# Optimization experiments

Hardware: AMD Instinct MI355X
Metric: run time of the kernel (lower is better)

## Reference

```python
import jax, jax.numpy as jnp
import numpy as np

B, S, E, H = 2, 2048, 1024, 16
HD = E // H  # head_dim = 64


def setup_inputs() -> dict:
    key = jax.random.key(0)
    k_x, k_wqkv, k_bqkv, k_wo, k_bo = jax.random.split(key, 5)
    # nn.Linear-style init scale ~ 1/sqrt(fan_in)
    s = 1.0 / np.sqrt(E)
    return {
        "x": jax.random.normal(k_x, (B, S, E), dtype=jnp.float32),
        "W_qkv": jax.random.uniform(k_wqkv, (3 * E, E), jnp.float32, -s, s),
        "b_qkv": jax.random.uniform(k_bqkv, (3 * E,), jnp.float32, -s, s),
        "W_out": jax.random.uniform(k_wo, (E, E), jnp.float32, -s, s),
        "b_out": jax.random.uniform(k_bo, (E,), jnp.float32, -s, s),
    }


def reference(x, W_qkv, b_qkv, W_out, b_out):
    # Fused QKV projection: (B,S,E) -> (B,S,3E)
    qkv = jnp.einsum("bse,fe->bsf", x, W_qkv) + b_qkv
    # Faithful to the torch code: reshape to (B,S,H,3*HD), then chunk last dim.
    qkv = qkv.reshape(B, S, H, 3 * HD)
    q, k, v = jnp.split(qkv, 3, axis=-1)  # each (B,S,H,HD)
    scale = 1.0 / jnp.sqrt(jnp.asarray(HD, dtype=x.dtype))
    # scores: (B,H,S,S)
    scores = jnp.einsum("bshd,bthd->bhst", q, k) * scale
    weights = jax.nn.softmax(scores, axis=-1)
    # context: (B,S,H,HD) -> (B,S,E)
    ctx = jnp.einsum("bhst,bthd->bshd", weights, v).reshape(B, S, E)
    return jnp.einsum("bse,fe->bsf", ctx, W_out) + b_out
```

## Files before the change

kernel.cpp:

```cpp
#include <hip/hip_runtime.h>
#include <hip/hip_bf16.h>

#define B_  2
#define S_  2048
#define E_  1024
#define H_  16
#define HD_ 64
#define T_  (B_*S_)
#define F_  (3*E_)

#define SW(r)  ((((r) & 7) << 4) ^ (((r) & 8) << 2))
#define SWV(r) (((((r) & 7) ^ (((r) >> 4) & 3)) << 4) ^ (((r) & 8) << 2))

using bf16 = __hip_bfloat16;
typedef __attribute__((ext_vector_type(8))) short bf16x8;
typedef __attribute__((ext_vector_type(4))) short short4v;
typedef __attribute__((ext_vector_type(4))) float f32x4;
typedef __attribute__((ext_vector_type(16))) float f32x16;
typedef __attribute__((ext_vector_type(4))) int i32x4;
typedef __attribute__((ext_vector_type(2))) unsigned int u32x2;

__device__ inline short f2bf(float x) {
  __hip_bfloat16 h = __float2bfloat16(x);
  return __builtin_bit_cast(short, h);
}
__device__ inline float bf2f(short x) {
  return __bfloat162float(__builtin_bit_cast(__hip_bfloat16, x));
}
__device__ inline int pk2(float lo, float hig) {
  return (int)((unsigned short)f2bf(lo) |
               ((unsigned int)(unsigned short)f2bf(hig) << 16));
}

__device__ inline void gload_lds16(const void* g, void* l) {
  __builtin_amdgcn_global_load_lds(
      (const __attribute__((address_space(1))) void*)g,
      (__attribute__((address_space(3))) void*)l, 16, 0, 0);
}

__global__ __launch_bounds__(256) void cvt_f32_bf16(
    const float* __restrict__ in, short* __restrict__ out, int n8) {
  int i = blockIdx.x * 256 + threadIdx.x;
  if (i >= n8) return;
  const float4* p = (const float4*)in + (size_t)i * 2;
  float4 a = p[0], b = p[1];
  bf16x8 r;
  r[0] = f2bf(a.x); r[1] = f2bf(a.y); r[2] = f2bf(a.z); r[3] = f2bf(a.w);
  r[4] = f2bf(b.x); r[5] = f2bf(b.y); r[6] = f2bf(b.z); r[7] = f2bf(b.w);
  *(bf16x8*)(out + (size_t)i * 8) = r;
}

__device__ inline void store_out(short* p, float v) { *p = f2bf(v); }
__device__ inline void store_out(float* p, float v) { *p = v; }

template<typename OutT>
__global__ __launch_bounds__(256) void gemm_nt(
    const short* __restrict__ A,
    const short* __restrict__ Bm,
    const float* __restrict__ bias,
    OutT* __restrict__ C,
    int M, int N, int K) {
  __shared__ __align__(16) char sAB[32768];
  char* sA = sAB;
  char* sB = sAB + 16384;
  const int tid  = threadIdx.x;
  const int w    = tid >> 6, lane = tid & 63;
  const int lr   = lane & 15, g = lane >> 4;
  const int brow = blockIdx.y * 128, bcol = blockIdx.x * 128;
  const int wr   = (w >> 1) * 64,  wc   = (w & 1) * 64;

  f32x4 acc[4][4];
  #pragma unroll
  for (int i = 0; i < 4; ++i)
    #pragma unroll
    for (int j = 0; j < 4; ++j) acc[i][j] = (f32x4)0.0f;

  const size_t Kb = (size_t)K * 2;
  const char* Ag = (const char*)A + (size_t)brow * Kb;
  const char* Bg = (const char*)Bm + (size_t)bcol * Kb;

  for (int k0 = 0; k0 < K; k0 += 64) {
    #pragma unroll
    for (int i = 0; i < 4; ++i) {
      int base = i * 4096 + w * 1024;
      int lb   = base + lane * 16;
      int r    = lb >> 7;
      int cb   = (lb & 127) ^ ((r & 7) << 4);
      gload_lds16(Ag + (size_t)r * Kb + (size_t)k0 * 2 + cb, sA + base);
      gload_lds16(Bg + (size_t)r * Kb + (size_t)k0 * 2 + cb, sB + base);
    }
    __syncthreads();
    #pragma unroll
    for (int ks = 0; ks < 2; ++ks) {
      bf16x8 af[4], bfr[4];
      #pragma unroll
      for (int m = 0; m < 4; ++m) {
        int row = wr + m * 16 + lr;
        int cb  = (ks * 64 + g * 16) ^ ((row & 7) << 4);
        af[m] = *(const bf16x8*)(sA + row * 128 + cb);
      }
      #pragma unroll
      for (int n = 0; n < 4; ++n) {
        int row = wc + n * 16 + lr;
        int cb  = (ks * 64 + g * 16) ^ ((row & 7) << 4);
        bfr[n] = *(const bf16x8*)(sB + row * 128 + cb);
      }
      #pragma unroll
      for (int m = 0; m < 4; ++m)
        #pragma unroll
        for (int n = 0; n < 4; ++n)
          acc[m][n] = __builtin_amdgcn_mfma_f32_16x16x32_bf16(
              af[m], bfr[n], acc[m][n], 0, 0, 0);
    }
    __syncthreads();
  }
  #pragma unroll
  for (int n = 0; n < 4; ++n) {
    int f = bcol + wc + n * 16 + lr;
    float bv = bias[f];
    #pragma unroll
    for (int m = 0; m < 4; ++m) {
      int t0 = brow + wr + m * 16 + g * 4;
      #pragma unroll
      for (int j = 0; j < 4; ++j) {
        store_out(&C[(size_t)(t0 + j) * N + f], acc[m][n][j] + bv);
      }
    }
  }
}

__global__ __launch_bounds__(256) void gemm_nt_n64(
    const short* __restrict__ A,
    const short* __restrict__ Bm,
    const float* __restrict__ bias,
    float* __restrict__ C,
    int M, int N, int K) {
  __shared__ __align__(16) char sAB[24576];
  char* sA = sAB;
  char* sB = sAB + 16384;
  const int tid  = threadIdx.x;
  const int w    = tid >> 6, lane = tid & 63;
  const int lr   = lane & 15, g = lane >> 4;
  const int brow = blockIdx.y * 128, bcol = blockIdx.x * 64;

  f32x4 acc[2][4];
  #pragma unroll
  for (int i = 0; i < 2; ++i)
    #pragma unroll
    for (int j = 0; j < 4; ++j) acc[i][j] = (f32x4)0.0f;

  const size_t Kb = (size_t)K * 2;
  const char* Ag = (const char*)A + (size_t)brow * Kb;
  const char* Bg = (const char*)Bm + (size_t)bcol * Kb;

  for (int k0 = 0; k0 < K; k0 += 64) {
    #pragma unroll
    for (int i = 0; i < 4; ++i) {
      int base = i * 4096 + w * 1024;
      int lb   = base + lane * 16;
      int r    = lb >> 7;
      int cb   = (lb & 127) ^ ((r & 7) << 4);
      gload_lds16(Ag + (size_t)r * Kb + (size_t)k0 * 2 + cb, sA + base);
    }
    #pragma unroll
    for (int i = 0; i < 2; ++i) {
      int base = i * 4096 + w * 1024;
      int lb   = base + lane * 16;
      int r    = lb >> 7;
      int cb   = (lb & 127) ^ ((r & 7) << 4);
      gload_lds16(Bg + (size_t)r * Kb + (size_t)k0 * 2 + cb, sB + base);
    }
    __syncthreads();
    #pragma unroll
    for (int ks = 0; ks < 2; ++ks) {
      bf16x8 af[2], bfr[4];
      #pragma unroll
      for (int m = 0; m < 2; ++m) {
        int row = w * 32 + m * 16 + lr;
        int cb  = (ks * 64 + g * 16) ^ ((row & 7) << 4);
        af[m] = *(const bf16x8*)(sA + row * 128 + cb);
      }
      #pragma unroll
      for (int n = 0; n < 4; ++n) {
        int row = n * 16 + lr;
        int cb  = (ks * 64 + g * 16) ^ ((row & 7) << 4);
        bfr[n] = *(const bf16x8*)(sB + row * 128 + cb);
      }
      #pragma unroll
      for (int m = 0; m < 2; ++m)
        #pragma unroll
        for (int n = 0; n < 4; ++n)
          acc[m][n] = __builtin_amdgcn_mfma_f32_16x16x32_bf16(
              af[m], bfr[n], acc[m][n], 0, 0, 0);
    }
    __syncthreads();
  }
  #pragma unroll
  for (int n = 0; n < 4; ++n) {
    int f = bcol + n * 16 + lr;
    float bv = bias[f];
    #pragma unroll
    for (int m = 0; m < 2; ++m) {
      int t0 = brow + w * 32 + m * 16 + g * 4;
      #pragma unroll
      for (int j = 0; j < 4; ++j) {
        C[(size_t)(t0 + j) * N + f] = acc[m][n][j] + bv;
      }
    }
  }
}

__global__ __launch_bounds__(256) void attn_kernel(
    const short* __restrict__ qkv, short* __restrict__ ctx) {
  __shared__ __align__(16) char smem[32768];
  const int tid = threadIdx.x;
  const int w = tid >> 6, lane = tid & 63;
  const int ql = lane & 31, hi = lane >> 5;
  const int qblk = blockIdx.x, h = blockIdx.y, b = blockIdx.z;

  const size_t rowB = (size_t)F_ * 2;
  const char* base = (const char*)qkv + (size_t)b * S_ * rowB + (size_t)h * 384;

  const int qrow = qblk * 128 + w * 32 + ql;
  const char* qp = base + (size_t)qrow * rowB;
  bf16x8 qf[4];
  #pragma unroll
  for (int ks = 0; ks < 4; ++ks) {
    bf16x8 t = *(const bf16x8*)(qp + ks * 32 + hi * 16);
    #pragma unroll
    for (int j = 0; j < 8; ++j) t[j] = f2bf(bf2f(t[j]) * 0.180336880f);
    qf[ks] = t;
  }

  const int vkg = tid >> 4;
  const int vfg = tid & 15;
  const int vkgp = (vkg & 12) | ((vkg & 1) << 1) | ((vkg >> 1) & 1);

  float l_run = 0.0f;
  f32x16 ot0 = (f32x16)0.0f, ot1 = (f32x16)0.0f;

#define STAGE_K(dstoff, srcb)                                           \
  do {                                                                  \
    _Pragma("unroll")                                                   \
    for (int i = 0; i < 2; ++i) {                                       \
      int lbase = i * 4096 + w * 1024;                                  \
      int lb = lbase + lane * 16;                                       \
      int r  = lb >> 7;                                                 \
      int cb = (lb & 127) ^ SW(r);                                      \
      gload_lds16((srcb) + (size_t)r * rowB + 128 + cb,                 \
                  smem + (dstoff) + lbase);                             \
    }                                                                   \
  } while (0)

#define LOAD_V(srcb)                                                    \
  do {                                                                  \
    const char* vp_ = (srcb) + 256 + vfg * 8;                           \
    nv0 = *(const short4v*)(vp_ + (size_t)(vkg * 4 + 0) * rowB);        \
    nv1 = *(const short4v*)(vp_ + (size_t)(vkg * 4 + 1) * rowB);        \
    nv2 = *(const short4v*)(vp_ + (size_t)(vkg * 4 + 2) * rowB);        \
    nv3 = *(const short4v*)(vp_ + (size_t)(vkg * 4 + 3) * rowB);        \
  } while (0)

#define WRITE_VT(dstoff)                                                \
  do {                                                                  \
    char* dvt_ = smem + (dstoff) + 8192;                                \
    _Pragma("unroll")                                                   \
    for (int f = 0; f < 4; ++f) {                                       \
      int fr = vfg * 4 + f;                                             \
      u32x2 dw;                                                         \
      dw[0] = (unsigned short)nv0[f] |                                  \
              ((unsigned int)(unsigned short)nv1[f] << 16);             \
      dw[1] = (unsigned short)nv2[f] |                                  \
              ((unsigned int)(unsigned short)nv3[f] << 16);             \
      *(u32x2*)(dvt_ + fr * 128 + ((vkgp * 8) ^ SWV(fr))) = dw;         \
    }                                                                   \
  } while (0)

  {
    short4v nv0, nv1, nv2, nv3;
    STAGE_K(0, base);
    LOAD_V(base);
    WRITE_VT(0);
  }
  __syncthreads();

  int cur = 0;
  for (int kt = 0; kt < 32; ++kt) {
    const int nxt = cur ^ 1;
    const char* sK  = smem + cur * 16384;
    const char* sVt = sK + 8192;

    short4v nv0, nv1, nv2, nv3;
    const char* nkvb = base + (size_t)((kt + 1) * 64) * rowB;
    if (kt < 31) {
      STAGE_K(nxt * 16384, nkvb);
      LOAD_V(nkvb);
    }

    f32x16 st0 = (f32x16)0.0f, st1 = (f32x16)0.0f;
    __builtin_amdgcn_s_setprio(1);
    #pragma unroll
    for (int ks = 0; ks < 4; ++ks) {
      int cb = (ks * 32 + hi * 16) ^ SW(ql);
      bf16x8 k0 = *(const bf16x8*)(sK + ql * 128 + cb);
      bf16x8 k1 = *(const bf16x8*)(sK + (ql + 32) * 128 + cb);
      st0 = __builtin_amdgcn_mfma_f32_32x32x16_bf16(k0, qf[ks], st0, 0, 0, 0);
      st1 = __builtin_amdgcn_mfma_f32_32x32x16_bf16(k1, qf[ks], st1, 0, 0, 0);
    }
    __builtin_amdgcn_s_setprio(0);

    float p0[16], p1[16];
    float rs = 0.0f;
    #pragma unroll
    for (int r = 0; r < 16; ++r) {
      p0[r] = exp2f(st0[r]);
      p1[r] = exp2f(st1[r]);
      rs += p0[r] + p1[r];
    }
    l_run += rs;

    i32x4 paw[4];
    #pragma unroll
    for (int q = 0; q < 4; ++q) {
      paw[0][q] = pk2(p0[2 * q], p0[2 * q + 1]);
      paw[1][q] = pk2(p0[8 + 2 * q], p0[9 + 2 * q]);
      paw[2][q] = pk2(p1[2 * q], p1[2 * q + 1]);
      paw[3][q] = pk2(p1[8 + 2 * q], p1[9 + 2 * q]);
    }

    __builtin_amdgcn_s_setprio(1);
    #pragma unroll
    for (int ks = 0; ks < 4; ++ks) {
      int cb = (ks * 32 + hi * 16);
      bf16x8 pf = __builtin_bit_cast(bf16x8, paw[ks]);
      bf16x8 v0 = *(const bf16x8*)(sVt + ql * 128 + (cb ^ SWV(ql)));
      bf16x8 v1 = *(const bf16x8*)(sVt + (ql + 32) * 128 + (cb ^ SWV(ql + 32)));
      ot0 = __builtin_amdgcn_mfma_f32_32x32x16_bf16(v0, pf, ot0, 0, 0, 0);
      ot1 = __builtin_amdgcn_mfma_f32_32x32x16_bf16(v1, pf, ot1, 0, 0, 0);
    }
    __builtin_amdgcn_s_setprio(0);

    if (kt < 31) {
      WRITE_VT(nxt * 16384);
    }
    __syncthreads();
    cur = nxt;
  }

  l_run += __shfl_xor(l_run, 32);
  float inv = 1.0f / l_run;
  short* crow = ctx + ((size_t)b * S_ + qrow) * E_ + h * 64;
  #pragma unroll
  for (int i = 0; i < 8; ++i) {
    int f0 = ((2 * i) & 3) + 8 * (i >> 1) + 4 * hi;
    int w0 = pk2(ot0[2 * i] * inv, ot0[2 * i + 1] * inv);
    int w1 = pk2(ot1[2 * i] * inv, ot1[2 * i + 1] * inv);
    *(int*)(crow + f0)      = w0;
    *(int*)(crow + f0 + 32) = w1;
  }
#undef STAGE_K
#undef LOAD_V
#undef WRITE_VT
}

extern "C" void kernel_launch(void* const* d_in, const int* in_sizes, int n_in,
                              void* d_out, int out_size, void* d_ws, size_t ws_size,
                              hipStream_t stream) {
  const float* x    = (const float*)d_in[0];
  const float* Wqkv = (const float*)d_in[1];
  const float* bqkv = (const float*)d_in[2];
  const float* Wout = (const float*)d_in[3];
  const float* bout = (const float*)d_in[4];

  char* ws = (char*)d_ws;
  short* xb    = (short*)(ws);
  short* wqkvb = (short*)(ws + 8388608);
  short* woutb = (short*)(ws + 8388608 + 6291456);
  short* qkvb  = (short*)(ws + 16777216);
  short* ctx   = (short*)(ws + 16777216 + 25165824);

  cvt_f32_bf16<<<2048, 256, 0, stream>>>(x, xb, (T_ * E_) / 8);
  cvt_f32_bf16<<<1536, 256, 0, stream>>>(Wqkv, wqkvb, (F_ * E_) / 8);
  cvt_f32_bf16<<<512, 256, 0, stream>>>(Wout, woutb, (E_ * E_) / 8);

  gemm_nt<short><<<dim3(F_ / 128, T_ / 128), 256, 0, stream>>>(
      xb, wqkvb, bqkv, qkvb, T_, F_, E_);

  attn_kernel<<<dim3(S_ / 128, H_, B_), 256, 0, stream>>>(qkvb, ctx);

  gemm_nt_n64<<<dim3(E_ / 64, T_ / 128), 256, 0, stream>>>(
      ctx, woutb, bout, (float*)d_out, T_, E_, E_);
}
```

Baseline: 212.9 us.

## Triple-buffer K/V in attention with explicit waitcnts and merge convert kernels

The attention kernel moves from double to triple buffering of K/V tiles in LDS (48KB). K is prefetched two tiles ahead via direct global-to-LDS loads and V one tile ahead, and __syncthreads is replaced with manual s_waitcnt vmcnt/lgkmcnt plus s_barrier so later loads can stay in flight across the barrier. Separately, the three fp32-to-bf16 conversion launches are merged into one kernel writing a contiguous workspace region. The larger LDS footprint may lower occupancy, and the hand-written waitcnt counts depend on exactly how many memory ops each macro issues, which the compiler does not check.

Measured after the change: 210.4 us. About the same (-1.2%).

```diff
diff --git a/kernel.cpp b/kernel.cpp
--- a/kernel.cpp
+++ b/kernel.cpp
@@ -38,11 +38,19 @@
       (__attribute__((address_space(3))) void*)l, 16, 0, 0);
 }
 
-__global__ __launch_bounds__(256) void cvt_f32_bf16(
-    const float* __restrict__ in, short* __restrict__ out, int n8) {
+#define NX8 ((T_*E_)/8)
+#define NW8 ((F_*E_)/8)
+#define NO8 ((E_*E_)/8)
+__global__ __launch_bounds__(256) void cvt_all(
+    const float* __restrict__ x, const float* __restrict__ wqkv,
+    const float* __restrict__ wout, short* __restrict__ out) {
   int i = blockIdx.x * 256 + threadIdx.x;
-  if (i >= n8) return;
-  const float4* p = (const float4*)in + (size_t)i * 2;
+  const float* src;
+  int off;
+  if (i < NX8)            { src = x;    off = i; }
+  else if (i < NX8 + NW8) { src = wqkv; off = i - NX8; }
+  else                    { src = wout; off = i - NX8 - NW8; }
+  const float4* p = (const float4*)src + (size_t)off * 2;
   float4 a = p[0], b = p[1];
   bf16x8 r;
   r[0] = f2bf(a.x); r[1] = f2bf(a.y); r[2] = f2bf(a.z); r[3] = f2bf(a.w);
@@ -212,7 +220,7 @@
 
 __global__ __launch_bounds__(256) void attn_kernel(
     const short* __restrict__ qkv, short* __restrict__ ctx) {
-  __shared__ __align__(16) char smem[32768];
+  __shared__ __align__(16) char smem[49152];
   const int tid = threadIdx.x;
   const int w = tid >> 6, lane = tid & 63;
   const int ql = lane & 31, hi = lane >> 5;
@@ -278,24 +286,25 @@
 
   {
     short4v nv0, nv1, nv2, nv3;
+    LOAD_V(base);
     STAGE_K(0, base);
-    LOAD_V(base);
+    STAGE_K(16384, base + (size_t)64 * rowB);
+    asm volatile("s_waitcnt vmcnt(2)" ::: "memory");
+    __builtin_amdgcn_sched_barrier(0);
     WRITE_VT(0);
-  }
-  __syncthreads();
-
-  int cur = 0;
+    asm volatile("s_waitcnt lgkmcnt(0)" ::: "memory");
+    __builtin_amdgcn_s_barrier();
+  }
+
   for (int kt = 0; kt < 32; ++kt) {
-    const int nxt = cur ^ 1;
+    const int cur = kt % 3;
     const char* sK  = smem + cur * 16384;
     const char* sVt = sK + 8192;
 
     short4v nv0, nv1, nv2, nv3;
-    const char* nkvb = base + (size_t)((kt + 1) * 64) * rowB;
-    if (kt < 31) {
-      STAGE_K(nxt * 16384, nkvb);
-      LOAD_V(nkvb);
-    }
+    if (kt < 31) LOAD_V(base + (size_t)((kt + 1) * 64) * rowB);
+    if (kt < 30) STAGE_K(((kt + 2) % 3) * 16384,
+                         base + (size_t)((kt + 2) * 64) * rowB);
 
     f32x16 st0 = (f32x16)0.0f, st1 = (f32x16)0.0f;
     __builtin_amdgcn_s_setprio(1);
@@ -341,10 +350,13 @@
     __builtin_amdgcn_s_setprio(0);
 
     if (kt < 31) {
-      WRITE_VT(nxt * 16384);
-    }
-    __syncthreads();
-    cur = nxt;
+      if (kt < 30) asm volatile("s_waitcnt vmcnt(2)" ::: "memory");
+      else         asm volatile("s_waitcnt vmcnt(0)" ::: "memory");
+      __builtin_amdgcn_sched_barrier(0);
+      WRITE_VT(((kt + 1) % 3) * 16384);
+      asm volatile("s_waitcnt lgkmcnt(0)" ::: "memory");
+      __builtin_amdgcn_s_barrier();
+    }
   }
 
   l_run += __shfl_xor(l_run, 32);
@@ -379,9 +391,7 @@
   short* qkvb  = (short*)(ws + 16777216);
   short* ctx   = (short*)(ws + 16777216 + 25165824);
 
-  cvt_f32_bf16<<<2048, 256, 0, stream>>>(x, xb, (T_ * E_) / 8);
-  cvt_f32_bf16<<<1536, 256, 0, stream>>>(Wqkv, wqkvb, (F_ * E_) / 8);
-  cvt_f32_bf16<<<512, 256, 0, stream>>>(Wout, woutb, (E_ * E_) / 8);
+  cvt_all<<<(NX8 + NW8 + NO8) / 256, 256, 0, stream>>>(x, Wqkv, Wout, xb);
 
   gemm_nt<short><<<dim3(F_ / 128, T_ / 128), 256, 0, stream>>>(
       xb, wqkvb, bqkv, qkvb, T_, F_, E_);
```
